# Optimization experiments

Measured on AMD Instinct MI355X. Metric: run time of the kernel, lower is better.

## Reference

```python
import jax, jax.numpy as jnp
import numpy as np

NUM_NODES = 8192
IN_FEATURES = 1024
OUT_FEATURES = 512
NUM_EDGES = 262144  # avg degree 32


def setup_inputs() -> dict:
    key = jax.random.key(0)
    k_x, k_w, k_b, k_src, k_dst = jax.random.split(key, 5)
    x = jax.random.normal(k_x, (NUM_NODES, IN_FEATURES), dtype=jnp.float32)
    # torch nn.Linear layout: weight [out, in], bias [out]
    W = jax.random.normal(k_w, (OUT_FEATURES, IN_FEATURES), dtype=jnp.float32) * (1.0 / np.sqrt(IN_FEATURES))
    b = jax.random.normal(k_b, (OUT_FEATURES,), dtype=jnp.float32) * 0.01
    src = jax.random.randint(k_src, (NUM_EDGES,), 0, NUM_NODES, dtype=jnp.int64)
    dst = jax.random.randint(k_dst, (NUM_EDGES,), 0, NUM_NODES, dtype=jnp.int64)
    edge_index = jnp.stack([src, dst], axis=0)
    return {"x": x, "W": W, "b": b, "edge_index": edge_index, "num_nodes": NUM_NODES}


def reference(x, W, b, edge_index, num_nodes):
    # Faithful to the torch module: build dense adjacency from edge list
    # (duplicate edges collapse to 1.0 via assignment semantics),
    # linear, (dropout p=0 -> identity), dense adj @ hidden, relu.
    adj = jnp.zeros((num_nodes, num_nodes), dtype=x.dtype)
    adj = adj.at[edge_index[0], edge_index[1]].set(1.0)
    hidden = x @ W.T + b            # [N, out]
    support = adj @ hidden          # [N, out] aggregation over neighbors
    return jax.nn.relu(support)
```

## Files before the change

kernel.cpp:

```cpp
#include <hip/hip_runtime.h>

#define N_NODES 8192
#define IN_F    1024
#define OUT_F   512
#define N_EDGES 262144
#define STRIDE  96

#define HID_OFF     0u
#define XB_OFF      8388608u
#define WB_OFF      25165824u
#define DEG_OFF     26214400u
#define COL_OFF     26247168u
#define MAX_DEG     STRIDE

typedef short  bf16x8 __attribute__((ext_vector_type(8)));
typedef float  f32x4  __attribute__((ext_vector_type(4)));

__device__ __forceinline__ unsigned short f2bf(float f) {
    unsigned u = __float_as_uint(f);
    u += 0x7fffu + ((u >> 16) & 1u);
    return (unsigned short)(u >> 16);
}

__device__ __forceinline__ float bflo(unsigned u) { return __uint_as_float(u << 16); }
__device__ __forceinline__ float bfhi(unsigned u) { return __uint_as_float(u & 0xffff0000u); }

__device__ __forceinline__ void ld_lds16(const void* g, void* l) {
    __builtin_amdgcn_global_load_lds(
        (const __attribute__((address_space(1))) void*)g,
        (__attribute__((address_space(3))) void*)l, 16, 0, 0);
}

#define NX8 (N_NODES * IN_F / 8)
#define NW8 (OUT_F * IN_F / 8)
__global__ __launch_bounds__(256) void cvt_bf16_all(const float* __restrict__ x,
                                                    const float* __restrict__ w,
                                                    unsigned short* __restrict__ xb,
                                                    int* __restrict__ deg) {
    int i = blockIdx.x * blockDim.x + threadIdx.x;
    if (i < N_NODES) deg[i] = 0;
    if (i >= NX8 + NW8) return;
    const float4* p = (i < NX8) ? ((const float4*)x + (size_t)i * 2)
                                : ((const float4*)w + (size_t)(i - NX8) * 2);
    float4 v0 = p[0], v1 = p[1];
    uint4 o;
    o.x = (unsigned)f2bf(v0.x) | ((unsigned)f2bf(v0.y) << 16);
    o.y = (unsigned)f2bf(v0.z) | ((unsigned)f2bf(v0.w) << 16);
    o.z = (unsigned)f2bf(v1.x) | ((unsigned)f2bf(v1.y) << 16);
    o.w = (unsigned)f2bf(v1.z) | ((unsigned)f2bf(v1.w) << 16);
    *((uint4*)xb + i) = o;
}

__global__ __launch_bounds__(256, 4) void gemm_scatter(const unsigned short* __restrict__ Xb,
                                                       const unsigned short* __restrict__ Wb,
                                                       const float* __restrict__ bias,
                                                       unsigned short* __restrict__ H,
                                                       const int* __restrict__ src,
                                                       const int* __restrict__ dst,
                                                       int* __restrict__ deg,
                                                       int* __restrict__ col) {
    __shared__ unsigned short As[64 * 32];
    __shared__ unsigned short Bs[64 * 32];

    const int bid = blockIdx.x;
    const int tid = threadIdx.x;

    if (bid >= 1024) {
        int e = (bid - 1024) * 256 + tid;
        int s = src[e];
        int slot = atomicAdd(&deg[s], 1);
        if (slot < STRIDE) col[s * STRIDE + slot] = dst[e];
        return;
    }

    const int lane = tid & 63;
    const int wave = tid >> 6;
    const int row0 = (bid & 127) * 64;
    const int col0 = (bid >> 7) * 64;
    const int wm   = (wave & 1) * 32;
    const int wn   = (wave >> 1) * 32;
    const int fm   = lane & 15;
    const int fk   = (lane >> 4) * 8;

    f32x4 acc[2][2];
#pragma unroll
    for (int i = 0; i < 2; ++i)
#pragma unroll
        for (int j = 0; j < 2; ++j) acc[i][j] = (f32x4)0.f;

    const int r0 = tid >> 2, kc0 = (tid & 3) * 8;

    for (int k0 = 0; k0 < IN_F; k0 += 32) {
        ld_lds16(Xb + (size_t)(row0 + r0) * IN_F + k0 + kc0, As + tid * 8);
        ld_lds16(Wb + (size_t)(col0 + r0) * IN_F + k0 + kc0, Bs + tid * 8);
        __syncthreads();

        bf16x8 a[2], b[2];
#pragma unroll
        for (int mi = 0; mi < 2; ++mi)
            a[mi] = *(const bf16x8*)&As[(wm + mi * 16 + fm) * 32 + fk];
#pragma unroll
        for (int ni = 0; ni < 2; ++ni)
            b[ni] = *(const bf16x8*)&Bs[(wn + ni * 16 + fm) * 32 + fk];
#pragma unroll
        for (int mi = 0; mi < 2; ++mi)
#pragma unroll
            for (int ni = 0; ni < 2; ++ni)
                acc[mi][ni] = __builtin_amdgcn_mfma_f32_16x16x32_bf16(
                    a[mi], b[ni], acc[mi][ni], 0, 0, 0);
        __syncthreads();
    }

    const int cm = (lane >> 4) * 4;
#pragma unroll
    for (int ni = 0; ni < 2; ++ni) {
        const int c = col0 + wn + ni * 16 + fm;
        const float bv = bias[c];
#pragma unroll
        for (int mi = 0; mi < 2; ++mi) {
#pragma unroll
            for (int r = 0; r < 4; ++r) {
                const int row = row0 + wm + mi * 16 + cm + r;
                H[(size_t)row * OUT_F + c] = f2bf(acc[mi][ni][r] + bv);
            }
        }
    }
}

__global__ __launch_bounds__(256) void aggregate(const unsigned short* __restrict__ H,
                                                 const int* __restrict__ dg,
                                                 const int* __restrict__ col,
                                                 float* __restrict__ out) {
    __shared__ int nbr[4][MAX_DEG];
    __shared__ int uniq[4][MAX_DEG];
    __shared__ int wcnt[4];
    const int wave = threadIdx.x >> 6;
    const int lane = threadIdx.x & 63;
    const int v    = blockIdx.x * 4 + wave;
    int d = dg[v];
    if (d > MAX_DEG) d = MAX_DEG;

    if (lane == 0) wcnt[wave] = 0;
    int id0 = -1, id1 = -1;
    if (lane < d)      { id0 = col[v * STRIDE + lane];      nbr[wave][lane]      = id0; }
    if (64 + lane < d) { id1 = col[v * STRIDE + 64 + lane]; nbr[wave][64 + lane] = id1; }
    __builtin_amdgcn_wave_barrier();

    bool k0 = (lane < d);
    const int lim0 = k0 ? lane : 0;
    for (int j = 0; j < lim0; ++j) k0 = k0 & (nbr[wave][j] != id0);
    bool k1 = (64 + lane < d);
    const int lim1 = k1 ? (64 + lane) : 0;
    for (int j = 0; j < lim1; ++j) k1 = k1 & (nbr[wave][j] != id1);
    if (k0) uniq[wave][atomicAdd(&wcnt[wave], 1)] = id0;
    if (k1) uniq[wave][atomicAdd(&wcnt[wave], 1)] = id1;
    __builtin_amdgcn_wave_barrier();
    const int n  = wcnt[wave];
    const int f0 = lane * 8;

    float a0=0,a1=0,a2=0,a3=0,a4=0,a5=0,a6=0,a7=0;
    int e = 0;
    for (; e + 4 <= n; e += 4) {
        const int i0 = uniq[wave][e], i1 = uniq[wave][e+1],
                  i2 = uniq[wave][e+2], i3 = uniq[wave][e+3];
        uint4 h0 = *(const uint4*)&H[(size_t)i0 * OUT_F + f0];
        uint4 h1 = *(const uint4*)&H[(size_t)i1 * OUT_F + f0];
        uint4 h2 = *(const uint4*)&H[(size_t)i2 * OUT_F + f0];
        uint4 h3 = *(const uint4*)&H[(size_t)i3 * OUT_F + f0];
        a0 += bflo(h0.x)+bflo(h1.x)+bflo(h2.x)+bflo(h3.x);
        a1 += bfhi(h0.x)+bfhi(h1.x)+bfhi(h2.x)+bfhi(h3.x);
        a2 += bflo(h0.y)+bflo(h1.y)+bflo(h2.y)+bflo(h3.y);
        a3 += bfhi(h0.y)+bfhi(h1.y)+bfhi(h2.y)+bfhi(h3.y);
        a4 += bflo(h0.z)+bflo(h1.z)+bflo(h2.z)+bflo(h3.z);
        a5 += bfhi(h0.z)+bfhi(h1.z)+bfhi(h2.z)+bfhi(h3.z);
        a6 += bflo(h0.w)+bflo(h1.w)+bflo(h2.w)+bflo(h3.w);
        a7 += bfhi(h0.w)+bfhi(h1.w)+bfhi(h2.w)+bfhi(h3.w);
    }
    for (; e < n; ++e) {
        uint4 h0 = *(const uint4*)&H[(size_t)uniq[wave][e] * OUT_F + f0];
        a0 += bflo(h0.x); a1 += bfhi(h0.x);
        a2 += bflo(h0.y); a3 += bfhi(h0.y);
        a4 += bflo(h0.z); a5 += bfhi(h0.z);
        a6 += bflo(h0.w); a7 += bfhi(h0.w);
    }
    float4 o0 = {fmaxf(a0,0.f), fmaxf(a1,0.f), fmaxf(a2,0.f), fmaxf(a3,0.f)};
    float4 o1 = {fmaxf(a4,0.f), fmaxf(a5,0.f), fmaxf(a6,0.f), fmaxf(a7,0.f)};
    *(float4*)&out[(size_t)v * OUT_F + f0]     = o0;
    *(float4*)&out[(size_t)v * OUT_F + f0 + 4] = o1;
}

extern "C" void kernel_launch(void* const* d_in, const int* in_sizes, int n_in,
                              void* d_out, int out_size, void* d_ws, size_t ws_size,
                              hipStream_t stream) {
    const float* x  = (const float*)d_in[0];
    const float* W  = (const float*)d_in[1];
    const float* b  = (const float*)d_in[2];
    const int*   ei = (const int*)d_in[3];
    float* out = (float*)d_out;

    char* ws = (char*)d_ws;
    unsigned short* H   = (unsigned short*)(ws + HID_OFF);
    unsigned short* Xb  = (unsigned short*)(ws + XB_OFF);
    unsigned short* Wb  = (unsigned short*)(ws + WB_OFF);
    int*            deg = (int*)(ws + DEG_OFF);
    int*            col = (int*)(ws + COL_OFF);

    cvt_bf16_all<<<(NX8 + NW8 + 255) / 256, 256, 0, stream>>>(x, W, Xb, deg);

    gemm_scatter<<<2048, 256, 0, stream>>>(Xb, Wb, b, H, ei, ei + N_EDGES, deg, col);

    aggregate<<<N_NODES / 4, 256, 0, stream>>>(H, deg, col, out);
}
```

Before: 139.5 us.

## Double GEMM K-tile with XOR-swizzled LDS and use nontemporal loads/stores

The GEMM k-loop now stages 64-wide K tiles instead of 32-wide, which halves the number of barrier pairs per output tile. LDS placement uses an XOR swizzle on 16-byte chunks to avoid bank conflicts when the MFMA fragments are read. The occupancy hint rises from 4 to 6 waves per SIMD. The fp32-to-bf16 conversion and the final output writes use nontemporal loads and stores to reduce cache pollution from streaming data. LDS per block doubles, and the nontemporal hints may interfere with L2 reuse.

```diff
diff --git a/kernel.cpp b/kernel.cpp
--- a/kernel.cpp
+++ b/kernel.cpp
@@ -40,9 +40,10 @@
     int i = blockIdx.x * blockDim.x + threadIdx.x;
     if (i < N_NODES) deg[i] = 0;
     if (i >= NX8 + NW8) return;
-    const float4* p = (i < NX8) ? ((const float4*)x + (size_t)i * 2)
-                                : ((const float4*)w + (size_t)(i - NX8) * 2);
-    float4 v0 = p[0], v1 = p[1];
+    const f32x4* p = (i < NX8) ? ((const f32x4*)x + (size_t)i * 2)
+                               : ((const f32x4*)w + (size_t)(i - NX8) * 2);
+    f32x4 v0 = __builtin_nontemporal_load(p);
+    f32x4 v1 = __builtin_nontemporal_load(p + 1);
     uint4 o;
     o.x = (unsigned)f2bf(v0.x) | ((unsigned)f2bf(v0.y) << 16);
     o.y = (unsigned)f2bf(v0.z) | ((unsigned)f2bf(v0.w) << 16);
@@ -51,7 +52,7 @@
     *((uint4*)xb + i) = o;
 }
 
-__global__ __launch_bounds__(256, 4) void gemm_scatter(const unsigned short* __restrict__ Xb,
+__global__ __launch_bounds__(256, 6) void gemm_scatter(const unsigned short* __restrict__ Xb,
                                                        const unsigned short* __restrict__ Wb,
                                                        const float* __restrict__ bias,
                                                        unsigned short* __restrict__ H,
@@ -59,8 +60,8 @@
                                                        const int* __restrict__ dst,
                                                        int* __restrict__ deg,
                                                        int* __restrict__ col) {
-    __shared__ unsigned short As[64 * 32];
-    __shared__ unsigned short Bs[64 * 32];
+    __shared__ unsigned short As[64 * 64];
+    __shared__ unsigned short Bs[64 * 64];
 
     const int bid = blockIdx.x;
     const int tid = threadIdx.x;
@@ -80,7 +81,8 @@
     const int wm   = (wave & 1) * 32;
     const int wn   = (wave >> 1) * 32;
     const int fm   = lane & 15;
-    const int fk   = (lane >> 4) * 8;
+    const int fm7  = fm & 7;
+    const int q    = lane >> 4;
 
     f32x4 acc[2][2];
 #pragma unroll
@@ -88,26 +90,33 @@
 #pragma unroll
         for (int j = 0; j < 2; ++j) acc[i][j] = (f32x4)0.f;
 
-    const int r0 = tid >> 2, kc0 = (tid & 3) * 8;
-
-    for (int k0 = 0; k0 < IN_F; k0 += 32) {
-        ld_lds16(Xb + (size_t)(row0 + r0) * IN_F + k0 + kc0, As + tid * 8);
-        ld_lds16(Wb + (size_t)(col0 + r0) * IN_F + k0 + kc0, Bs + tid * 8);
+    const int r0 = tid >> 3;
+    const int kp = ((tid & 7) ^ (r0 & 7)) * 8;
+
+    for (int k0 = 0; k0 < IN_F; k0 += 64) {
+        ld_lds16(Xb + (size_t)(row0 + r0) * IN_F + k0 + kp,      As + tid * 8);
+        ld_lds16(Xb + (size_t)(row0 + r0 + 32) * IN_F + k0 + kp, As + (tid + 256) * 8);
+        ld_lds16(Wb + (size_t)(col0 + r0) * IN_F + k0 + kp,      Bs + tid * 8);
+        ld_lds16(Wb + (size_t)(col0 + r0 + 32) * IN_F + k0 + kp, Bs + (tid + 256) * 8);
         __syncthreads();
 
-        bf16x8 a[2], b[2];
-#pragma unroll
-        for (int mi = 0; mi < 2; ++mi)
-            a[mi] = *(const bf16x8*)&As[(wm + mi * 16 + fm) * 32 + fk];
-#pragma unroll
-        for (int ni = 0; ni < 2; ++ni)
-            b[ni] = *(const bf16x8*)&Bs[(wn + ni * 16 + fm) * 32 + fk];
-#pragma unroll
-        for (int mi = 0; mi < 2; ++mi)
+#pragma unroll
+        for (int s = 0; s < 2; ++s) {
+            const int kq = s * 4 + q;
+            bf16x8 a[2], b[2];
+#pragma unroll
+            for (int mi = 0; mi < 2; ++mi)
+                a[mi] = *(const bf16x8*)&As[(((wm + mi * 16 + fm) << 3) + (kq ^ fm7)) << 3];
 #pragma unroll
             for (int ni = 0; ni < 2; ++ni)
-                acc[mi][ni] = __builtin_amdgcn_mfma_f32_16x16x32_bf16(
-                    a[mi], b[ni], acc[mi][ni], 0, 0, 0);
+                b[ni] = *(const bf16x8*)&Bs[(((wn + ni * 16 + fm) << 3) + (kq ^ fm7)) << 3];
+#pragma unroll
+            for (int mi = 0; mi < 2; ++mi)
+#pragma unroll
+                for (int ni = 0; ni < 2; ++ni)
+                    acc[mi][ni] = __builtin_amdgcn_mfma_f32_16x16x32_bf16(
+                        a[mi], b[ni], acc[mi][ni], 0, 0, 0);
+        }
         __syncthreads();
     }
 
@@ -183,10 +192,10 @@
         a4 += bflo(h0.z); a5 += bfhi(h0.z);
         a6 += bflo(h0.w); a7 += bfhi(h0.w);
     }
-    float4 o0 = {fmaxf(a0,0.f), fmaxf(a1,0.f), fmaxf(a2,0.f), fmaxf(a3,0.f)};
-    float4 o1 = {fmaxf(a4,0.f), fmaxf(a5,0.f), fmaxf(a6,0.f), fmaxf(a7,0.f)};
-    *(float4*)&out[(size_t)v * OUT_F + f0]     = o0;
-    *(float4*)&out[(size_t)v * OUT_F + f0 + 4] = o1;
+    f32x4 o0 = {fmaxf(a0,0.f), fmaxf(a1,0.f), fmaxf(a2,0.f), fmaxf(a3,0.f)};
+    f32x4 o1 = {fmaxf(a4,0.f), fmaxf(a5,0.f), fmaxf(a6,0.f), fmaxf(a7,0.f)};
+    __builtin_nontemporal_store(o0, (f32x4*)&out[(size_t)v * OUT_F + f0]);
+    __builtin_nontemporal_store(o1, (f32x4*)&out[(size_t)v * OUT_F + f0 + 4]);
 }
 
 extern "C" void kernel_launch(void* const* d_in, const int* in_sizes, int n_in,
```

Result: no change. 139.2 us (-0.3%).

## Enlarge GEMM tile to 128x128 and use nontemporal loads/stores

Applied to the files above, without the earlier changes.

The GEMM block tile grows from 64x64 to 128x128, with each wave computing a 64x64 sub-tile of 4x4 MFMA fragments. This raises data reuse per LDS load and cuts the GEMM block count from 1024 to 256. The conversion kernel now uses nontemporal loads and drops its bounds check, and the aggregate kernel writes its output with nontemporal stores. The trade-offs are higher register pressure and only 256 GEMM blocks to fill the device.

```diff
diff --git a/kernel.cpp b/kernel.cpp
--- a/kernel.cpp
+++ b/kernel.cpp
@@ -16,10 +16,10 @@
 typedef short  bf16x8 __attribute__((ext_vector_type(8)));
 typedef float  f32x4  __attribute__((ext_vector_type(4)));
 
-__device__ __forceinline__ unsigned short f2bf(float f) {
+__device__ __forceinline__ unsigned f2bf(float f) {
     unsigned u = __float_as_uint(f);
     u += 0x7fffu + ((u >> 16) & 1u);
-    return (unsigned short)(u >> 16);
+    return u >> 16;
 }
 
 __device__ __forceinline__ float bflo(unsigned u) { return __uint_as_float(u << 16); }
@@ -33,21 +33,21 @@
 
 #define NX8 (N_NODES * IN_F / 8)
 #define NW8 (OUT_F * IN_F / 8)
-__global__ __launch_bounds__(256) void cvt_bf16_all(const float* __restrict__ x,
-                                                    const float* __restrict__ w,
-                                                    unsigned short* __restrict__ xb,
-                                                    int* __restrict__ deg) {
+__global__ __launch_bounds__(256) void cvt_all(const float* __restrict__ x,
+                                               const float* __restrict__ w,
+                                               unsigned short* __restrict__ xb,
+                                               int* __restrict__ deg) {
     int i = blockIdx.x * blockDim.x + threadIdx.x;
     if (i < N_NODES) deg[i] = 0;
-    if (i >= NX8 + NW8) return;
-    const float4* p = (i < NX8) ? ((const float4*)x + (size_t)i * 2)
-                                : ((const float4*)w + (size_t)(i - NX8) * 2);
-    float4 v0 = p[0], v1 = p[1];
+    const f32x4* p = (i < NX8) ? ((const f32x4*)x + (size_t)i * 2)
+                               : ((const f32x4*)w + (size_t)(i - NX8) * 2);
+    f32x4 v0 = __builtin_nontemporal_load(p);
+    f32x4 v1 = __builtin_nontemporal_load(p + 1);
     uint4 o;
-    o.x = (unsigned)f2bf(v0.x) | ((unsigned)f2bf(v0.y) << 16);
-    o.y = (unsigned)f2bf(v0.z) | ((unsigned)f2bf(v0.w) << 16);
-    o.z = (unsigned)f2bf(v1.x) | ((unsigned)f2bf(v1.y) << 16);
-    o.w = (unsigned)f2bf(v1.z) | ((unsigned)f2bf(v1.w) << 16);
+    o.x = f2bf(v0.x) | (f2bf(v0.y) << 16);
+    o.y = f2bf(v0.z) | (f2bf(v0.w) << 16);
+    o.z = f2bf(v1.x) | (f2bf(v1.y) << 16);
+    o.w = f2bf(v1.z) | (f2bf(v1.w) << 16);
     *((uint4*)xb + i) = o;
 }
 
@@ -59,14 +59,14 @@
                                                        const int* __restrict__ dst,
                                                        int* __restrict__ deg,
                                                        int* __restrict__ col) {
-    __shared__ unsigned short As[64 * 32];
-    __shared__ unsigned short Bs[64 * 32];
+    __shared__ unsigned short As[128 * 32];
+    __shared__ unsigned short Bs[128 * 32];
 
     const int bid = blockIdx.x;
     const int tid = threadIdx.x;
 
-    if (bid >= 1024) {
-        int e = (bid - 1024) * 256 + tid;
+    if (bid >= 256) {
+        int e = (bid - 256) * 256 + tid;
         int s = src[e];
         int slot = atomicAdd(&deg[s], 1);
         if (slot < STRIDE) col[s * STRIDE + slot] = dst[e];
@@ -75,37 +75,40 @@
 
     const int lane = tid & 63;
     const int wave = tid >> 6;
-    const int row0 = (bid & 127) * 64;
-    const int col0 = (bid >> 7) * 64;
-    const int wm   = (wave & 1) * 32;
-    const int wn   = (wave >> 1) * 32;
+    const int row0 = (bid & 63) * 128;
+    const int col0 = (bid >> 6) * 128;
+    const int wm   = (wave & 1) * 64;
+    const int wn   = (wave >> 1) * 64;
     const int fm   = lane & 15;
     const int fk   = (lane >> 4) * 8;
 
-    f32x4 acc[2][2];
-#pragma unroll
-    for (int i = 0; i < 2; ++i)
-#pragma unroll
-        for (int j = 0; j < 2; ++j) acc[i][j] = (f32x4)0.f;
+    f32x4 acc[4][4];
+#pragma unroll
+    for (int i = 0; i < 4; ++i)
+#pragma unroll
+        for (int j = 0; j < 4; ++j) acc[i][j] = (f32x4)0.f;
 
     const int r0 = tid >> 2, kc0 = (tid & 3) * 8;
+    const int r1 = r0 + 64;
 
     for (int k0 = 0; k0 < IN_F; k0 += 32) {
         ld_lds16(Xb + (size_t)(row0 + r0) * IN_F + k0 + kc0, As + tid * 8);
         ld_lds16(Wb + (size_t)(col0 + r0) * IN_F + k0 + kc0, Bs + tid * 8);
+        ld_lds16(Xb + (size_t)(row0 + r1) * IN_F + k0 + kc0, As + (tid + 256) * 8);
+        ld_lds16(Wb + (size_t)(col0 + r1) * IN_F + k0 + kc0, Bs + (tid + 256) * 8);
         __syncthreads();
 
-        bf16x8 a[2], b[2];
-#pragma unroll
-        for (int mi = 0; mi < 2; ++mi)
+        bf16x8 a[4], b[4];
+#pragma unroll
+        for (int mi = 0; mi < 4; ++mi)
             a[mi] = *(const bf16x8*)&As[(wm + mi * 16 + fm) * 32 + fk];
 #pragma unroll
-        for (int ni = 0; ni < 2; ++ni)
+        for (int ni = 0; ni < 4; ++ni)
             b[ni] = *(const bf16x8*)&Bs[(wn + ni * 16 + fm) * 32 + fk];
 #pragma unroll
-        for (int mi = 0; mi < 2; ++mi)
-#pragma unroll
-            for (int ni = 0; ni < 2; ++ni)
+        for (int mi = 0; mi < 4; ++mi)
+#pragma unroll
+            for (int ni = 0; ni < 4; ++ni)
                 acc[mi][ni] = __builtin_amdgcn_mfma_f32_16x16x32_bf16(
                     a[mi], b[ni], acc[mi][ni], 0, 0, 0);
         __syncthreads();
@@ -113,15 +116,15 @@
 
     const int cm = (lane >> 4) * 4;
 #pragma unroll
-    for (int ni = 0; ni < 2; ++ni) {
+    for (int ni = 0; ni < 4; ++ni) {
         const int c = col0 + wn + ni * 16 + fm;
         const float bv = bias[c];
 #pragma unroll
-        for (int mi = 0; mi < 2; ++mi) {
+        for (int mi = 0; mi < 4; ++mi) {
 #pragma unroll
             for (int r = 0; r < 4; ++r) {
                 const int row = row0 + wm + mi * 16 + cm + r;
-                H[(size_t)row * OUT_F + c] = f2bf(acc[mi][ni][r] + bv);
+                H[(size_t)row * OUT_F + c] = (unsigned short)f2bf(acc[mi][ni][r] + bv);
             }
         }
     }
@@ -183,10 +186,10 @@
         a4 += bflo(h0.z); a5 += bfhi(h0.z);
         a6 += bflo(h0.w); a7 += bfhi(h0.w);
     }
-    float4 o0 = {fmaxf(a0,0.f), fmaxf(a1,0.f), fmaxf(a2,0.f), fmaxf(a3,0.f)};
-    float4 o1 = {fmaxf(a4,0.f), fmaxf(a5,0.f), fmaxf(a6,0.f), fmaxf(a7,0.f)};
-    *(float4*)&out[(size_t)v * OUT_F + f0]     = o0;
-    *(float4*)&out[(size_t)v * OUT_F + f0 + 4] = o1;
+    f32x4 o0 = {fmaxf(a0,0.f), fmaxf(a1,0.f), fmaxf(a2,0.f), fmaxf(a3,0.f)};
+    f32x4 o1 = {fmaxf(a4,0.f), fmaxf(a5,0.f), fmaxf(a6,0.f), fmaxf(a7,0.f)};
+    __builtin_nontemporal_store(o0, (f32x4*)&out[(size_t)v * OUT_F + f0]);
+    __builtin_nontemporal_store(o1, (f32x4*)&out[(size_t)v * OUT_F + f0 + 4]);
 }
 
 extern "C" void kernel_launch(void* const* d_in, const int* in_sizes, int n_in,
@@ -201,13 +204,13 @@
     char* ws = (char*)d_ws;
     unsigned short* H   = (unsigned short*)(ws + HID_OFF);
     unsigned short* Xb  = (unsigned short*)(ws + XB_OFF);
-    unsigned short* Wb  = (unsigned short*)(ws + WB_OFF);
     int*            deg = (int*)(ws + DEG_OFF);
     int*            col = (int*)(ws + COL_OFF);
 
-    cvt_bf16_all<<<(NX8 + NW8 + 255) / 256, 256, 0, stream>>>(x, W, Xb, deg);
-
-    gemm_scatter<<<2048, 256, 0, stream>>>(Xb, Wb, b, H, ei, ei + N_EDGES, deg, col);
+    cvt_all<<<(NX8 + NW8) / 256, 256, 0, stream>>>(x, W, Xb, deg);
+
+    gemm_scatter<<<256 + 1024, 256, 0, stream>>>(Xb, (unsigned short*)(ws + WB_OFF),
+                                                 b, H, ei, ei + N_EDGES, deg, col);
 
     aggregate<<<N_NODES / 4, 256, 0, stream>>>(H, deg, col, out);
 }
```

After: 144.9 us. +3.8%, slower.
